# Optimization experiments

Hardware: AMD Instinct MI355X
Metric: run time of the kernel (lower is better)

The kernel has to match this reference:

```python
import jax, jax.numpy as jnp
import numpy as np


def setup_inputs() -> dict:
    key = jax.random.key(0)
    k1, _ = jax.random.split(key)
    x = jax.random.normal(k1, (2, 16, 16, 16, 64), dtype=jnp.float32)
    gamma = jnp.ones((1,), dtype=jnp.float32)  # learned scalar (zeros at init; ones to make output nontrivial)
    return {"x": x, "gamma": gamma}


def reference(x, gamma):
    # x: (B, D, H, W, C); faithful to the Keras layer: flatten spatial dims,
    # energy = Q @ Q^T over the N=D*H*W axis, softmax(axis=-1), attn @ Q,
    # then gamma-scaled residual add.
    B, D, H, W, C = x.shape
    N = D * H * W
    q = x.reshape(B, N, C)                            # proj_query (B, N, C)
    energy = jnp.einsum('bnc,bmc->bnm', q, q)          # (B, N, N)
    attn = jax.nn.softmax(energy, axis=-1)
    out = jnp.einsum('bnm,bmc->bnc', attn, q)          # (B, N, C)
    out = out.reshape(B, D, H, W, C)
    return gamma * out + x
```

## Files before the change

kernel.cpp:

```cpp
#include <hip/hip_runtime.h>
#include <hip/hip_bf16.h>
#include <math.h>


#define NN 4096
#define CC 64
#define LOG2E 1.4426950408889634f

typedef __attribute__((ext_vector_type(4))) float f32x4;
typedef __attribute__((ext_vector_type(8))) short bf16x8;
typedef __attribute__((ext_vector_type(4))) short bf16x4;
typedef unsigned short u16;
typedef __attribute__((ext_vector_type(4))) u16 u16x4;

__device__ inline u16 f2bf(float f) {
  union { float f; unsigned u; } v; v.f = f;
  unsigned r = (v.u + 0x7fffu + ((v.u >> 16) & 1u)) >> 16;
  return (u16)r;
}
__device__ inline u16 f2bf_t(float f) {
  union { float f; unsigned u; } v; v.f = f;
  return (u16)(v.u >> 16);
}
__device__ inline float bf2f(short h) {
  union { unsigned u; float f; } v;
  v.u = ((unsigned)(unsigned short)h) << 16;
  return v.f;
}
__device__ inline bf16x8 cvt8(f32x4 a, f32x4 b) {
  bf16x8 r;
  r[0] = (short)f2bf(a[0]); r[1] = (short)f2bf(a[1]);
  r[2] = (short)f2bf(a[2]); r[3] = (short)f2bf(a[3]);
  r[4] = (short)f2bf(b[0]); r[5] = (short)f2bf(b[1]);
  r[6] = (short)f2bf(b[2]); r[7] = (short)f2bf(b[3]);
  return r;
}

__global__ __launch_bounds__(256) void prep_kernel(const float* __restrict__ x,
                                                   u16* __restrict__ Qb,
                                                   u16* __restrict__ Vt) {
  __shared__ u16 t[64][36];
  int b = blockIdx.x >> 7;
  int n0 = (blockIdx.x & 127) << 5;
  const f32x4* x4 = (const f32x4*)(x + ((size_t)b * NN + n0) * CC);
  u16* qb = Qb + ((size_t)b * NN + n0) * CC;
#pragma unroll
  for (int j = 0; j < 2; ++j) {
    int idx4 = j * 256 + threadIdx.x;
    int i = idx4 >> 4, cg = idx4 & 15;
    f32x4 v = x4[idx4];
    u16x4 h;
    h[0] = f2bf(v[0]); h[1] = f2bf(v[1]); h[2] = f2bf(v[2]); h[3] = f2bf(v[3]);
    *(u16x4*)(qb + (size_t)i * CC + cg * 4) = h;
    t[cg * 4 + 0][i] = h[0]; t[cg * 4 + 1][i] = h[1];
    t[cg * 4 + 2][i] = h[2]; t[cg * 4 + 3][i] = h[3];
  }
  __syncthreads();
  int kb = n0 >> 6, kw0 = n0 & 63;
#pragma unroll
  for (int j = 0; j < 2; ++j) {
    int idx4 = j * 256 + threadIdx.x;
    int c = idx4 >> 3, i4 = (idx4 & 7) * 4;
    u16x4 h = *(const u16x4*)(&t[c][i4]);
    *(u16x4*)(Vt + (((size_t)b * (NN / 64) + kb) * 64 + c) * 64 + kw0 + i4) = h;
  }
}

template <int S>
__global__ __launch_bounds__(256, 2) void attn_split(
    const u16* __restrict__ Qb, const u16* __restrict__ Vt,
    u16* __restrict__ Opart, float* __restrict__ lpart) {
  constexpr int KPS = NN / S;
  constexpr int ITERS = KPS / 64;
  const int w = threadIdx.x >> 6;
  const int lane = threadIdx.x & 63;
  const int quad = lane >> 4, col = lane & 15;
  const int blk = blockIdx.x;
  const int b = blk / (32 * S);
  const int rb = (blk / S) & 31;
  const int s = blk % S;

  __shared__ u16 KT[2][64 * 68];
  __shared__ u16 VT[2][64 * 68];
  __shared__ u16 PB[4][16 * 68];

  const u16* Qbase = Qb + (size_t)b * NN * CC;
  const u16* Vbase = Vt + (size_t)b * NN * CC;
  const int row0 = rb * 128 + w * 32;

  bf16x8 qs0[2], qs1[2];
  float m_i[2][4];
#pragma unroll
  for (int rt = 0; rt < 2; ++rt) {
    const u16* qp = Qbase + (size_t)(row0 + rt * 16 + col) * CC + quad * 8;
    bf16x8 r0 = *(const bf16x8*)qp;
    bf16x8 r1 = *(const bf16x8*)(qp + 32);
    float msum = 0.f;
#pragma unroll
    for (int j = 0; j < 8; ++j) {
      float a0 = bf2f(r0[j]), a1 = bf2f(r1[j]);
      u16 h0 = f2bf(a0 * LOG2E), h1 = f2bf(a1 * LOG2E);
      qs0[rt][j] = (short)h0; qs1[rt][j] = (short)h1;
      msum += bf2f((short)h0) * a0 + bf2f((short)h1) * a1;
    }
    msum += __shfl_xor(msum, 16);
    msum += __shfl_xor(msum, 32);
#pragma unroll
    for (int r = 0; r < 4; ++r) m_i[rt][r] = __shfl(msum, quad * 4 + r);
  }

  f32x4 zero = {0.f, 0.f, 0.f, 0.f};
  f32x4 acc[2][4] = {{zero, zero, zero, zero}, {zero, zero, zero, zero}};
  float l_i[2][4] = {{0.f, 0.f, 0.f, 0.f}, {0.f, 0.f, 0.f, 0.f}};

  const int srow = w * 16 + (lane >> 3);
  const int sj = lane & 7;
  bf16x8 stK0, stK1, stV0, stV1;

  auto issue_loads = [&](int kt0) {
    const u16* ks = Qbase + (size_t)(kt0 + srow) * CC + sj * 8;
    stK0 = *(const bf16x8*)ks;
    stK1 = *(const bf16x8*)(ks + 8 * CC);
    const u16* vs = Vbase + ((size_t)(kt0 >> 6)) * 4096 + srow * 64 + sj * 8;
    stV0 = *(const bf16x8*)vs;
    stV1 = *(const bf16x8*)(vs + 8 * 64);
  };
  auto write_tile = [&](int p) {
    *(bf16x8*)(&KT[p][srow * 68 + sj * 8]) = stK0;
    *(bf16x8*)(&KT[p][(srow + 8) * 68 + sj * 8]) = stK1;
    *(bf16x8*)(&VT[p][srow * 68 + sj * 8]) = stV0;
    *(bf16x8*)(&VT[p][(srow + 8) * 68 + sj * 8]) = stV1;
  };

  issue_loads(s * KPS);
  write_tile(0);
  for (int i = 0; i < ITERS; ++i) {
    __syncthreads();
    const int p = i & 1;
    if (i + 1 < ITERS) issue_loads(s * KPS + (i + 1) * 64);
    bf16x8 ka[4], kb_[4], va[4], vb[4];
#pragma unroll
    for (int t = 0; t < 4; ++t) {
      ka[t] = *(const bf16x8*)(&KT[p][(t * 16 + col) * 68 + quad * 8]);
      kb_[t] = *(const bf16x8*)(&KT[p][(t * 16 + col) * 68 + 32 + quad * 8]);
      va[t] = *(const bf16x8*)(&VT[p][(t * 16 + col) * 68 + quad * 8]);
      vb[t] = *(const bf16x8*)(&VT[p][(t * 16 + col) * 68 + 32 + quad * 8]);
    }
#pragma unroll
    for (int rt = 0; rt < 2; ++rt) {
      f32x4 sx[4];
#pragma unroll
      for (int t = 0; t < 4; ++t) {
        sx[t] = __builtin_amdgcn_mfma_f32_16x16x32_bf16(qs0[rt], ka[t], zero, 0, 0, 0);
        sx[t] = __builtin_amdgcn_mfma_f32_16x16x32_bf16(qs1[rt], kb_[t], sx[t], 0, 0, 0);
      }
#pragma unroll
      for (int t = 0; t < 4; ++t) {
#pragma unroll
        for (int r = 0; r < 4; ++r) {
          float pv = exp2f(sx[t][r] - m_i[rt][r]);
          l_i[rt][r] += pv;
          PB[w][(quad * 4 + r) * 68 + t * 16 + col] = f2bf_t(pv);
        }
      }
      bf16x8 pf0 = *(const bf16x8*)(&PB[w][col * 68 + quad * 8]);
      bf16x8 pf1 = *(const bf16x8*)(&PB[w][col * 68 + 32 + quad * 8]);
#pragma unroll
      for (int cg = 0; cg < 4; ++cg) {
        acc[rt][cg] = __builtin_amdgcn_mfma_f32_16x16x32_bf16(pf0, va[cg], acc[rt][cg], 0, 0, 0);
        acc[rt][cg] = __builtin_amdgcn_mfma_f32_16x16x32_bf16(pf1, vb[cg], acc[rt][cg], 0, 0, 0);
      }
    }
    if (i + 1 < ITERS) write_tile(p ^ 1);
  }

#pragma unroll
  for (int rt = 0; rt < 2; ++rt)
#pragma unroll
    for (int r = 0; r < 4; ++r)
#pragma unroll
      for (int off = 1; off < 16; off <<= 1)
        l_i[rt][r] += __shfl_xor(l_i[rt][r], off, 16);

  size_t pbase = (((size_t)b * 32 + rb) * S + s) * 128 * 64;
#pragma unroll
  for (int rt = 0; rt < 2; ++rt) {
#pragma unroll
    for (int r = 0; r < 4; ++r) {
      int lr = w * 32 + rt * 16 + quad * 4 + r;
      size_t o = pbase + (size_t)lr * 64;
      Opart[o + col]      = f2bf(acc[rt][0][r]);
      Opart[o + col + 16] = f2bf(acc[rt][1][r]);
      Opart[o + col + 32] = f2bf(acc[rt][2][r]);
      Opart[o + col + 48] = f2bf(acc[rt][3][r]);
      if (col == 0)
        lpart[(((size_t)b * 32 + rb) * S + s) * 128 + lr] = l_i[rt][r];
    }
  }
}

template <int S>
__global__ __launch_bounds__(256) void epi_kernel(
    const float* __restrict__ x, const float* __restrict__ gamma,
    const u16* __restrict__ Opart, const float* __restrict__ lpart,
    float* __restrict__ out) {
  int idx = blockIdx.x * 256 + threadIdx.x;
  int c = idx & 63;
  int n = (idx >> 6) & (NN - 1);
  int b = idx >> 18;
  int rb = n >> 7, lr = n & 127;
  size_t base = ((size_t)b * 32 + rb) * S;
  float sO = 0.f, sL = 0.f;
#pragma unroll
  for (int s = 0; s < S; ++s) {
    sO += bf2f((short)Opart[((base + s) * 128 + lr) * 64 + c]);
    sL += lpart[(base + s) * 128 + lr];
  }
  out[idx] = gamma[0] * (sO / sL) + x[idx];
}

template <int WPB>
__global__ __launch_bounds__(WPB * 64, 4) void attn_fast(
    const float* __restrict__ x, const float* __restrict__ gamma,
    const u16* __restrict__ Qb, const u16* __restrict__ Vt,
    float* __restrict__ out) {
  const int w = threadIdx.x >> 6;
  const int lane = threadIdx.x & 63;
  const int quad = lane >> 4, col = lane & 15;
  const int b = blockIdx.x >> 8;
  const int tile = (blockIdx.x & 255) << 4;

  extern __shared__ char smem[];
  float* Osh = (float*)smem;
  float* lsh = Osh + WPB * 1024;
  u16* pl = (u16*)(lsh + WPB * 16) + w * 2176;

  const size_t xoff = (size_t)b * NN * CC;
  const u16* Qbase = Qb + xoff;
  const u16* Vbase = Vt + xoff;

  bf16x8 qf0 = *(const bf16x8*)(Qbase + (size_t)(tile + col) * CC + quad * 8);
  bf16x8 qf1 = *(const bf16x8*)(Qbase + (size_t)(tile + col) * CC + 32 + quad * 8);

  float msum = 0.f;
#pragma unroll
  for (int j = 0; j < 8; ++j) {
    float a = bf2f(qf0[j]), c = bf2f(qf1[j]);
    msum += a * a + c * c;
  }
  msum += __shfl_xor(msum, 16);
  msum += __shfl_xor(msum, 32);
  float m_i[4];
#pragma unroll
  for (int r = 0; r < 4; ++r) m_i[r] = __shfl(msum, quad * 4 + r);

  f32x4 zero = {0.f, 0.f, 0.f, 0.f};
  f32x4 acc[4] = {zero, zero, zero, zero};
  float l_i[4] = {0.f, 0.f, 0.f, 0.f};

  const int k0 = w * (NN / WPB);
#pragma unroll 2
  for (int kt = k0; kt < k0 + NN / WPB; kt += 64) {
    u16* plc = pl + ((kt >> 6) & 1) * 1088;
    f32x4 sx[4];
#pragma unroll
    for (int t = 0; t < 4; ++t) {
      const u16* kp = Qbase + (size_t)(kt + t * 16 + col) * CC + quad * 8;
      bf16x8 ka = *(const bf16x8*)kp;
      bf16x8 kb = *(const bf16x8*)(kp + 32);
      sx[t] = __builtin_amdgcn_mfma_f32_16x16x32_bf16(qf0, ka, zero, 0, 0, 0);
      sx[t] = __builtin_amdgcn_mfma_f32_16x16x32_bf16(qf1, kb, sx[t], 0, 0, 0);
    }
#pragma unroll
    for (int t = 0; t < 4; ++t) {
#pragma unroll
      for (int r = 0; r < 4; ++r) {
        float p = __expf(sx[t][r] - m_i[r]);
        l_i[r] += p;
        plc[(quad * 4 + r) * 68 + t * 16 + col] = f2bf(p);
      }
    }
    bf16x8 pf0 = *(const bf16x8*)(plc + col * 68 + quad * 8);
    bf16x8 pf1 = *(const bf16x8*)(plc + col * 68 + 32 + quad * 8);
#pragma unroll
    for (int cg = 0; cg < 4; ++cg) {
      const u16* vp = Vbase + (((size_t)(kt >> 6)) * 64 + cg * 16 + col) * 64 + quad * 8;
      bf16x8 v0 = *(const bf16x8*)vp;
      bf16x8 v1 = *(const bf16x8*)(vp + 32);
      acc[cg] = __builtin_amdgcn_mfma_f32_16x16x32_bf16(pf0, v0, acc[cg], 0, 0, 0);
      acc[cg] = __builtin_amdgcn_mfma_f32_16x16x32_bf16(pf1, v1, acc[cg], 0, 0, 0);
    }
  }

#pragma unroll
  for (int r = 0; r < 4; ++r)
#pragma unroll
    for (int off = 1; off < 16; off <<= 1) l_i[r] += __shfl_xor(l_i[r], off, 16);
#pragma unroll
  for (int r = 0; r < 4; ++r) {
    int row = quad * 4 + r;
    Osh[(w * 16 + row) * 64 + col]      = acc[0][r];
    Osh[(w * 16 + row) * 64 + col + 16] = acc[1][r];
    Osh[(w * 16 + row) * 64 + col + 32] = acc[2][r];
    Osh[(w * 16 + row) * 64 + col + 48] = acc[3][r];
    if (col == 0) lsh[w * 16 + row] = l_i[r];
  }
  __syncthreads();

  float g = gamma[0];
  for (int row = w; row < 16; row += WPB) {
    float L = 0.f, val = 0.f;
#pragma unroll
    for (int w2 = 0; w2 < WPB; ++w2) {
      L += lsh[w2 * 16 + row];
      val += Osh[(w2 * 16 + row) * 64 + lane];
    }
    size_t o = xoff + (size_t)(tile + row) * CC + lane;
    out[o] = g * (val / L) + x[o];
  }
}

template <int WPB>
__global__ __launch_bounds__(512) void attn_fb(const float* __restrict__ x,
                                               const float* __restrict__ gamma,
                                               float* __restrict__ out) {
  const int w = threadIdx.x >> 6;
  const int lane = threadIdx.x & 63;
  const int quad = lane >> 4, col = lane & 15;
  const int b = blockIdx.x >> 8;
  const int tile = (blockIdx.x & 255) << 4;

  extern __shared__ char smem[];
  float* Osh = (float*)smem;
  float* msh = Osh + WPB * 1024;
  float* lsh = msh + WPB * 16;
  u16* pl = (u16*)(lsh + WPB * 16) + w * 768;
  u16* vt = (u16*)(lsh + WPB * 16) + WPB * 768 + w * 2176;

  const size_t xoff = (size_t)b * NN * CC;
  const f32x4* x4 = (const f32x4*)(x + xoff);

  bf16x8 qf0, qf1;
  {
    int ri = (tile + col) * 16 + quad * 2;
    qf0 = cvt8(x4[ri], x4[ri + 1]);
    qf1 = cvt8(x4[ri + 8], x4[ri + 9]);
  }
  f32x4 zero = {0.f, 0.f, 0.f, 0.f};
  f32x4 acc0 = zero, acc1 = zero, acc2 = zero, acc3 = zero;
  float m_i[4], l_i[4];
#pragma unroll
  for (int r = 0; r < 4; ++r) { m_i[r] = -1e30f; l_i[r] = 0.f; }

  const int k0 = w * (NN / WPB);
  for (int kt = k0; kt < k0 + NN / WPB; kt += 32) {
    bf16x8 k00, k01, k10, k11;
    {
      int kb = (kt + col) * 16 + quad * 2;
      k00 = cvt8(x4[kb], x4[kb + 1]);
      k01 = cvt8(x4[kb + 8], x4[kb + 9]);
      k10 = cvt8(x4[kb + 256], x4[kb + 257]);
      k11 = cvt8(x4[kb + 264], x4[kb + 265]);
#pragma unroll
      for (int h = 0; h < 2; ++h) {
        bf16x8 va = h ? k10 : k00, vb = h ? k11 : k01;
        int base = (h * 16 + col) * 68 + quad * 8;
        *(bf16x4*)(vt + base) = __builtin_shufflevector(va, va, 0, 1, 2, 3);
        *(bf16x4*)(vt + base + 4) = __builtin_shufflevector(va, va, 4, 5, 6, 7);
        *(bf16x4*)(vt + base + 32) = __builtin_shufflevector(vb, vb, 0, 1, 2, 3);
        *(bf16x4*)(vt + base + 36) = __builtin_shufflevector(vb, vb, 4, 5, 6, 7);
      }
    }
    f32x4 s0 = zero, s1 = zero;
    s0 = __builtin_amdgcn_mfma_f32_16x16x32_bf16(qf0, k00, s0, 0, 0, 0);
    s0 = __builtin_amdgcn_mfma_f32_16x16x32_bf16(qf1, k01, s0, 0, 0, 0);
    s1 = __builtin_amdgcn_mfma_f32_16x16x32_bf16(qf0, k10, s1, 0, 0, 0);
    s1 = __builtin_amdgcn_mfma_f32_16x16x32_bf16(qf1, k11, s1, 0, 0, 0);

    float p0[4], p1[4], alpha[4];
#pragma unroll
    for (int r = 0; r < 4; ++r) {
      float mx = fmaxf(s0[r], s1[r]);
#pragma unroll
      for (int off = 1; off < 16; off <<= 1) mx = fmaxf(mx, __shfl_xor(mx, off, 16));
      float mn = fmaxf(m_i[r], mx);
      alpha[r] = __expf(m_i[r] - mn);
      p0[r] = __expf(s0[r] - mn);
      p1[r] = __expf(s1[r] - mn);
      float rs = p0[r] + p1[r];
#pragma unroll
      for (int off = 1; off < 16; off <<= 1) rs += __shfl_xor(rs, off, 16);
      l_i[r] = l_i[r] * alpha[r] + rs;
      m_i[r] = mn;
    }
#pragma unroll
    for (int r = 0; r < 4; ++r) {
      acc0[r] *= alpha[r]; acc1[r] *= alpha[r];
      acc2[r] *= alpha[r]; acc3[r] *= alpha[r];
    }
#pragma unroll
    for (int r = 0; r < 4; ++r) {
      pl[(quad * 4 + r) * 24 + col] = f2bf(p0[r]);
      pl[384 + (quad * 4 + r) * 24 + col] = f2bf(p1[r]);
    }
    bf16x8 pf = *(const bf16x8*)(pl + (quad >> 1) * 384 + col * 24 + (quad & 1) * 8);

    bf16x8 v0, v1, v2, v3;
#pragma unroll
    for (int j = 0; j < 8; ++j) {
      int rb = (quad * 8 + j) * 68 + col;
      v0[j] = (short)vt[rb];
      v1[j] = (short)vt[rb + 16];
      v2[j] = (short)vt[rb + 32];
      v3[j] = (short)vt[rb + 48];
    }
    acc0 = __builtin_amdgcn_mfma_f32_16x16x32_bf16(pf, v0, acc0, 0, 0, 0);
    acc1 = __builtin_amdgcn_mfma_f32_16x16x32_bf16(pf, v1, acc1, 0, 0, 0);
    acc2 = __builtin_amdgcn_mfma_f32_16x16x32_bf16(pf, v2, acc2, 0, 0, 0);
    acc3 = __builtin_amdgcn_mfma_f32_16x16x32_bf16(pf, v3, acc3, 0, 0, 0);
  }

#pragma unroll
  for (int r = 0; r < 4; ++r) {
    int row = quad * 4 + r;
    Osh[(w * 16 + row) * 64 + col] = acc0[r];
    Osh[(w * 16 + row) * 64 + col + 16] = acc1[r];
    Osh[(w * 16 + row) * 64 + col + 32] = acc2[r];
    Osh[(w * 16 + row) * 64 + col + 48] = acc3[r];
    if (col == 0) { msh[w * 16 + row] = m_i[r]; lsh[w * 16 + row] = l_i[r]; }
  }
  __syncthreads();

  float g = gamma[0];
  for (int row = w; row < 16; row += WPB) {
    float M = -1e30f;
#pragma unroll
    for (int w2 = 0; w2 < WPB; ++w2) M = fmaxf(M, msh[w2 * 16 + row]);
    float L = 0.f, val = 0.f;
#pragma unroll
    for (int w2 = 0; w2 < WPB; ++w2) {
      float e = __expf(msh[w2 * 16 + row] - M);
      L += lsh[w2 * 16 + row] * e;
      val += Osh[(w2 * 16 + row) * 64 + lane] * e;
    }
    size_t o = xoff + (size_t)(tile + row) * CC + lane;
    out[o] = g * (val / L) + x[o];
  }
}

extern "C" void kernel_launch(void* const* d_in, const int* in_sizes, int n_in,
                              void* d_out, int out_size, void* d_ws, size_t ws_size,
                              hipStream_t stream) {
  const float* x = (const float*)d_in[0];
  const float* gamma = (const float*)d_in[1];
  float* out = (float*)d_out;

  constexpr int S = 8;
  constexpr size_t kQV = (size_t)2 * 2 * NN * CC * sizeof(u16);
  constexpr size_t kOp = (size_t)2 * 32 * S * 128 * 64 * sizeof(u16);
  constexpr size_t kLp = (size_t)2 * 32 * S * 128 * sizeof(float);
  if (ws_size >= kQV + kOp + kLp) {
    u16* Qb = (u16*)d_ws;
    u16* Vt = Qb + (size_t)2 * NN * CC;
    u16* Opart = (u16*)((char*)d_ws + kQV);
    float* lpart = (float*)((char*)d_ws + kQV + kOp);
    prep_kernel<<<256, 256, 0, stream>>>(x, Qb, Vt);
    attn_split<S><<<2 * 32 * S, 256, 0, stream>>>(Qb, Vt, Opart, lpart);
    epi_kernel<S><<<(2 * NN * CC) / 256, 256, 0, stream>>>(x, gamma, Opart, lpart, out);
  } else if (ws_size >= kQV) {
    u16* Qb = (u16*)d_ws;
    u16* Vt = Qb + (size_t)2 * NN * CC;
    prep_kernel<<<256, 256, 0, stream>>>(x, Qb, Vt);
    constexpr int SM = 8 * 1024 * 4 + 8 * 16 * 4 + 8 * 2176 * 2;
    attn_fast<8><<<512, 512, SM, stream>>>(x, gamma, Qb, Vt, out);
  } else {
    constexpr int SM4 = 4 * (1024 + 32) * 4 + 4 * 768 * 2 + 4 * 2176 * 2;
    attn_fb<4><<<512, 256, SM4, stream>>>(x, gamma, out);
  }
}
```

Measured before the change: 85.46 us.

## Double split-K factor, vectorize epilogue, shrink prep tiles, unroll attention loop

Raises the split factor S from 8 to 16, so the split attention kernel launches twice as many blocks with half the key range each. The epilogue now handles four channels per thread with vector loads and stores, and the prep kernel uses 16-row tiles across twice as many blocks. The main attention loop is also fully unrolled. The intent is better GPU occupancy and fewer memory transactions, at the cost of twice the partial-output traffic and more code size and register pressure.

```diff
diff --git a/kernel.cpp b/kernel.cpp
--- a/kernel.cpp
+++ b/kernel.cpp
@@ -39,14 +39,13 @@
 __global__ __launch_bounds__(256) void prep_kernel(const float* __restrict__ x,
                                                    u16* __restrict__ Qb,
                                                    u16* __restrict__ Vt) {
-  __shared__ u16 t[64][36];
-  int b = blockIdx.x >> 7;
-  int n0 = (blockIdx.x & 127) << 5;
+  __shared__ u16 t[64][20];
+  int b = blockIdx.x >> 8;
+  int n0 = (blockIdx.x & 255) << 4;
   const f32x4* x4 = (const f32x4*)(x + ((size_t)b * NN + n0) * CC);
   u16* qb = Qb + ((size_t)b * NN + n0) * CC;
-#pragma unroll
-  for (int j = 0; j < 2; ++j) {
-    int idx4 = j * 256 + threadIdx.x;
+  {
+    int idx4 = threadIdx.x;
     int i = idx4 >> 4, cg = idx4 & 15;
     f32x4 v = x4[idx4];
     u16x4 h;
@@ -57,10 +56,9 @@
   }
   __syncthreads();
   int kb = n0 >> 6, kw0 = n0 & 63;
-#pragma unroll
-  for (int j = 0; j < 2; ++j) {
-    int idx4 = j * 256 + threadIdx.x;
-    int c = idx4 >> 3, i4 = (idx4 & 7) * 4;
+  {
+    int idx4 = threadIdx.x;
+    int c = idx4 >> 2, i4 = (idx4 & 3) * 4;
     u16x4 h = *(const u16x4*)(&t[c][i4]);
     *(u16x4*)(Vt + (((size_t)b * (NN / 64) + kb) * 64 + c) * 64 + kw0 + i4) = h;
   }
@@ -134,6 +132,7 @@
 
   issue_loads(s * KPS);
   write_tile(0);
+#pragma unroll
   for (int i = 0; i < ITERS; ++i) {
     __syncthreads();
     const int p = i & 1;
@@ -204,19 +203,29 @@
     const float* __restrict__ x, const float* __restrict__ gamma,
     const u16* __restrict__ Opart, const float* __restrict__ lpart,
     float* __restrict__ out) {
-  int idx = blockIdx.x * 256 + threadIdx.x;
-  int c = idx & 63;
-  int n = (idx >> 6) & (NN - 1);
-  int b = idx >> 18;
+  int t = blockIdx.x * 256 + threadIdx.x;
+  int cg = t & 15;
+  int n = (t >> 4) & (NN - 1);
+  int b = t >> 16;
   int rb = n >> 7, lr = n & 127;
-  size_t base = ((size_t)b * 32 + rb) * S;
-  float sO = 0.f, sL = 0.f;
+  size_t obase = (((size_t)b * 32 + rb) * S) * 128 * 64 + (size_t)lr * 64 + cg * 4;
+  size_t lbase = (((size_t)b * 32 + rb) * S) * 128 + lr;
+  f32x4 sO = {0.f, 0.f, 0.f, 0.f};
+  float sL = 0.f;
 #pragma unroll
   for (int s = 0; s < S; ++s) {
-    sO += bf2f((short)Opart[((base + s) * 128 + lr) * 64 + c]);
-    sL += lpart[(base + s) * 128 + lr];
-  }
-  out[idx] = gamma[0] * (sO / sL) + x[idx];
+    u16x4 o4 = *(const u16x4*)(Opart + obase + (size_t)s * 128 * 64);
+    sL += lpart[lbase + s * 128];
+    sO[0] += bf2f((short)o4[0]); sO[1] += bf2f((short)o4[1]);
+    sO[2] += bf2f((short)o4[2]); sO[3] += bf2f((short)o4[3]);
+  }
+  size_t xi = (((size_t)b * NN + n) * CC + cg * 4);
+  f32x4 xv = *(const f32x4*)(x + xi);
+  float g = gamma[0], inv = 1.f / sL;
+  f32x4 ov;
+#pragma unroll
+  for (int j = 0; j < 4; ++j) ov[j] = g * (sO[j] * inv) + xv[j];
+  *(f32x4*)(((float*)out) + xi) = ov;
 }
 
 template <int WPB>
@@ -455,7 +464,7 @@
   const float* gamma = (const float*)d_in[1];
   float* out = (float*)d_out;
 
-  constexpr int S = 8;
+  constexpr int S = 16;
   constexpr size_t kQV = (size_t)2 * 2 * NN * CC * sizeof(u16);
   constexpr size_t kOp = (size_t)2 * 32 * S * 128 * 64 * sizeof(u16);
   constexpr size_t kLp = (size_t)2 * 32 * S * 128 * sizeof(float);
@@ -464,13 +473,13 @@
     u16* Vt = Qb + (size_t)2 * NN * CC;
     u16* Opart = (u16*)((char*)d_ws + kQV);
     float* lpart = (float*)((char*)d_ws + kQV + kOp);
-    prep_kernel<<<256, 256, 0, stream>>>(x, Qb, Vt);
+    prep_kernel<<<512, 256, 0, stream>>>(x, Qb, Vt);
     attn_split<S><<<2 * 32 * S, 256, 0, stream>>>(Qb, Vt, Opart, lpart);
-    epi_kernel<S><<<(2 * NN * CC) / 256, 256, 0, stream>>>(x, gamma, Opart, lpart, out);
+    epi_kernel<S><<<(2 * NN * 16) / 256, 256, 0, stream>>>(x, gamma, Opart, lpart, out);
   } else if (ws_size >= kQV) {
     u16* Qb = (u16*)d_ws;
     u16* Vt = Qb + (size_t)2 * NN * CC;
-    prep_kernel<<<256, 256, 0, stream>>>(x, Qb, Vt);
+    prep_kernel<<<512, 256, 0, stream>>>(x, Qb, Vt);
     constexpr int SM = 8 * 1024 * 4 + 8 * 16 * 4 + 8 * 2176 * 2;
     attn_fast<8><<<512, 512, SM, stream>>>(x, gamma, Qb, Vt, out);
   } else {
```

Result: slower. 90.09 us (+5.4%).
